# Optimization experiments

Measured on AMD Instinct MI355X. Metric: run time of the kernel, lower is better.

The kernel has to match this reference:

```python
import jax, jax.numpy as jnp
import numpy as np
import math

H = 16
D_MODEL = 1024
D_K = D_MODEL // H


def setup_inputs() -> dict:
    key = jax.random.key(0)
    ks = jax.random.split(key, 11)
    B, S = 2, 2048
    scale = 1.0 / math.sqrt(D_MODEL)
    inp = {
        "query": jax.random.normal(ks[0], (B, S, D_MODEL), dtype=jnp.float32),
        "key": jax.random.normal(ks[1], (B, S, D_MODEL), dtype=jnp.float32),
        "value": jax.random.normal(ks[2], (B, S, D_MODEL), dtype=jnp.float32),
        # torch nn.Linear convention: W is [out_features, in_features]
        "Wq": jax.random.normal(ks[3], (D_MODEL, D_MODEL), dtype=jnp.float32) * scale,
        "bq": jnp.zeros((D_MODEL,), dtype=jnp.float32),
        "Wk": jax.random.normal(ks[4], (D_MODEL, D_MODEL), dtype=jnp.float32) * scale,
        "bk": jnp.zeros((D_MODEL,), dtype=jnp.float32),
        "Wv": jax.random.normal(ks[5], (D_MODEL, D_MODEL), dtype=jnp.float32) * scale,
        "bv": jnp.zeros((D_MODEL,), dtype=jnp.float32),
        "Wo": jax.random.normal(ks[6], (D_MODEL, D_MODEL), dtype=jnp.float32) * scale,
        "bo": jnp.zeros((D_MODEL,), dtype=jnp.float32),
    }
    return inp


def _split_heads(x):
    # [b, s, h*d_k] -> [b, h, s, d_k]
    b, s, _ = x.shape
    return x.reshape(b, s, H, D_K).transpose(0, 2, 1, 3)


def reference(query, key, value, Wq, bq, Wk, bk, Wv, bv, Wo, bo):
    q = _split_heads(query @ Wq.T + bq)
    k = _split_heads(key @ Wk.T + bk)
    v = _split_heads(value @ Wv.T + bv)
    # scaled dot-product attention, full L x L scores per head
    scores = jnp.einsum("bhqd,bhkd->bhqk", q, k) / math.sqrt(D_K)
    attn = jax.nn.softmax(scores, axis=-1)
    ctx = jnp.einsum("bhqk,bhkd->bhqd", attn, v)  # [b, h, s, d_k]
    b, h, s, d = ctx.shape
    ctx = ctx.transpose(0, 2, 1, 3).reshape(b, s, h * d)
    return ctx @ Wo.T + bo
```

## Files before the change

kernel.cpp:

```cpp
#include <hip/hip_runtime.h>

typedef unsigned int u32;
typedef unsigned short u16;
typedef __attribute__((ext_vector_type(8))) short short8;
typedef __attribute__((ext_vector_type(4))) float f32x4;
typedef __attribute__((ext_vector_type(2))) u32 u32x2;
typedef __attribute__((ext_vector_type(4))) u32 u32x4;

#define DEV __device__ __forceinline__

DEV u16 f2bf(float f) {
  u32 u = __builtin_bit_cast(u32, f);
  u = (u + 0x7FFFu + ((u >> 16) & 1u)) >> 16;
  return (u16)u;
}

DEV float fexp2(float x) {
#if __has_builtin(__builtin_amdgcn_exp2f)
  return __builtin_amdgcn_exp2f(x);
#else
  return exp2f(x);
#endif
}

DEV u32 cvt_pk_bf16(float lo, float hi) {
  u32 r;
  asm("v_cvt_pk_bf16_f32 %0, %1, %2" : "=v"(r) : "v"(lo), "v"(hi));
  return r;
}

DEV void llds16(const void* g, void* lds) {
  __builtin_amdgcn_global_load_lds(
      (const __attribute__((address_space(1))) u32*)g,
      (__attribute__((address_space(3))) u32*)lds, 16, 0, 0);
}

struct CvtArgs {
  const float* src[7];
  u16* dst[7];
};

__global__ void cvt_all(CvtArgs ca) {
  int i = blockIdx.x * blockDim.x + threadIdx.x;
  int chunk = i >> 17;
  int seg = chunk < 12 ? (chunk >> 2) : (chunk - 9);
  u32 base8 = (seg < 3) ? (u32)seg * 524288u : 1572864u + ((u32)seg - 3) * 131072u;
  size_t off = ((size_t)i - base8) * 8;
  const f32x4* p = (const f32x4*)(ca.src[seg] + off);
  f32x4 a = p[0], b = p[1];
  short8 o;
  o[0] = (short)f2bf(a[0]); o[1] = (short)f2bf(a[1]);
  o[2] = (short)f2bf(a[2]); o[3] = (short)f2bf(a[3]);
  o[4] = (short)f2bf(b[0]); o[5] = (short)f2bf(b[1]);
  o[6] = (short)f2bf(b[2]); o[7] = (short)f2bf(b[3]);
  *(short8*)(ca.dst[seg] + off) = o;
}

struct GemmArgs {
  const u16* A[3];
  const u16* W[3];
  const float* bias[3];
  void* C[3];
  float scale[3];
};

template <int BM, int BN, int WAVES_M, int OUT_BF16, int NB_M>
__global__ __launch_bounds__(256, 2) void gemm_bt(GemmArgs ga) {
  constexpr int K = 1024, N = 1024;
  constexpr int WAVES_N = 4 / WAVES_M;
  constexpr int WM = BM / WAVES_M, WN = BN / WAVES_N;
  constexpr int AM = WM / 16, AN = WN / 16;
  constexpr int SEGS = (BM + BN) / 16;
  constexpr int PW = SEGS / 4;

  __shared__ u16 lsA[BM * 32];
  __shared__ u16 lsB[BN * 32];

  const u32 orig = blockIdx.x;
  const u32 nid = (orig & 7u) * (gridDim.x >> 3) + (orig >> 3);
  const int bn = (int)(nid & 7u);
  const int bm = (int)((nid >> 3) % (u32)NB_M);
  const int z = (int)((nid >> 3) / (u32)NB_M);

  const u16* __restrict__ A = ga.A[z];
  const u16* __restrict__ W = ga.W[z];
  const int tid = threadIdx.x;
  const int l = tid & 63, w = tid >> 6;
  const int lg = l >> 4, lr = l & 15;
  const int wm = w / WAVES_N, wn = w % WAVES_N;

  f32x4 acc[AM][AN];
#pragma unroll
  for (int i = 0; i < AM; ++i)
#pragma unroll
    for (int j = 0; j < AN; ++j) acc[i][j] = (f32x4){0.f, 0.f, 0.f, 0.f};

  for (int k0 = 0; k0 < K; k0 += 32) {
    __syncthreads();
#pragma unroll
    for (int i = 0; i < PW; ++i) {
      int s = w * PW + i;
      if (s < BM / 16) {
        u32 sb = s * 1024;
        u32 lb = sb + l * 16;
        u32 row = lb >> 6, colS = (lb & 63) >> 1;
        llds16(A + (size_t)(bm * BM + row) * K + k0 + colS, (char*)lsA + sb);
      } else {
        u32 sb = (u32)(s - BM / 16) * 1024;
        u32 lb = sb + l * 16;
        u32 row = lb >> 6, colS = (lb & 63) >> 1;
        llds16(W + (size_t)(bn * BN + row) * K + k0 + colS, (char*)lsB + sb);
      }
    }
    __syncthreads();
    short8 af[AM], bf[AN];
#pragma unroll
    for (int i = 0; i < AM; ++i)
      af[i] = *(const short8*)&lsA[(wm * WM + i * 16 + lr) * 32 + lg * 8];
#pragma unroll
    for (int j = 0; j < AN; ++j)
      bf[j] = *(const short8*)&lsB[(wn * WN + j * 16 + lr) * 32 + lg * 8];
#pragma unroll
    for (int i = 0; i < AM; ++i)
#pragma unroll
      for (int j = 0; j < AN; ++j)
        acc[i][j] = __builtin_amdgcn_mfma_f32_16x16x32_bf16(af[i], bf[j], acc[i][j], 0, 0, 0);
  }

  const float sc = ga.scale[z];
  const float* __restrict__ bias = ga.bias[z];
#pragma unroll
  for (int j = 0; j < AN; ++j) {
    int col = bn * BN + wn * WN + j * 16 + lr;
    float bv = bias[col];
#pragma unroll
    for (int i = 0; i < AM; ++i) {
      int row0 = bm * BM + wm * WM + i * 16 + lg * 4;
#pragma unroll
      for (int r = 0; r < 4; ++r) {
        float v = (acc[i][j][r] + bv) * sc;
        if constexpr (OUT_BF16)
          ((u16*)ga.C[z])[(size_t)(row0 + r) * N + col] = f2bf(v);
        else
          ((float*)ga.C[z])[(size_t)(row0 + r) * N + col] = v;
      }
    }
  }
}

__global__ __launch_bounds__(256, 2) void attn_fwd(
    const u16* __restrict__ Q, const u16* __restrict__ Kp,
    const u16* __restrict__ V, u16* __restrict__ O) {
  constexpr int S = 2048, LD = 1024;
  __shared__ u16 Kt[4][64 * 64];
  __shared__ u16 Vt[4][64 * 64];
  const int tid = threadIdx.x;
  const int l = tid & 63, w = tid >> 6;
  const int lg = l >> 4, lr = l & 15;

  const u32 orig = blockIdx.x;
  const u32 nid = (orig & 7u) * 64u + (orig >> 3);
  const int qt = (int)(nid & 15u);
  const int h = (int)((nid >> 4) & 15u);
  const int b = (int)(nid >> 8);

  const size_t base = ((size_t)b * S) * LD + h * 64;
  const int q0 = qt * 128 + w * 32;

  short8 qf[2][2];
#pragma unroll
  for (int g = 0; g < 2; ++g)
#pragma unroll
    for (int c = 0; c < 2; ++c)
      qf[g][c] = *(const short8*)&Q[base + (size_t)(q0 + g * 16 + lr) * LD + c * 32 + lg * 8];

  f32x4 acc[2][4];
#pragma unroll
  for (int g = 0; g < 2; ++g)
#pragma unroll
    for (int i = 0; i < 4; ++i) acc[g][i] = (f32x4){0.f, 0.f, 0.f, 0.f};
  float lsum[2] = {0.f, 0.f};

  const int m = tid & 31;
  const int kp0 = m * 2;
  const int key0 = ((m & 16) << 1) + ((m & 2) << 3) + (((m >> 2) & 3) << 2) + ((m & 1) << 1);
  const int vd0 = (tid >> 5) * 8;

#define KSTAGE(T)                                                               \
  {                                                                             \
    _Pragma("unroll") for (int i_ = 0; i_ < 2; ++i_) {                          \
      u32 sb = (u32)(w * 2 + i_) * 1024;                                        \
      u32 lb = sb + l * 16;                                                     \
      u32 key = lb >> 7;                                                        \
      u32 inner = (lb & 127) ^ ((key & 7) << 4);                                \
      llds16(Kp + base + (size_t)((T) * 64 + key) * LD + (inner >> 1),          \
             (char*)Kt[(T) & 3] + sb);                                          \
    }                                                                           \
  }
#define VLOAD(T, VA, VB)                                                        \
  {                                                                             \
    VA = *(const short8*)&V[base + (size_t)((T) * 64 + key0) * LD + vd0];       \
    VB = *(const short8*)&V[base + (size_t)((T) * 64 + key0 + 1) * LD + vd0];   \
  }
#define VWRITE(T, VA, VB)                                                       \
  {                                                                             \
    _Pragma("unroll") for (int jj = 0; jj < 8; ++jj) {                          \
      u32 pv = (u32)(u16)(VA)[jj] | ((u32)(u16)(VB)[jj] << 16);                 \
      u32 addr = (u32)((vd0 + jj) * 128 + kp0 * 2) ^ ((u32)jj << 4);            \
      *(u32*)((char*)Vt[(T) & 3] + addr) = pv;                                  \
    }                                                                           \
  }
#define QK(T, SV)                                                               \
  {                                                                             \
    __builtin_amdgcn_s_setprio(1);                                              \
    _Pragma("unroll") for (int ks = 0; ks < 4; ++ks) {                          \
      u32 a0 = (u32)(((ks * 16 + lr) * 128 + lg * 16) ^ ((lr & 7) << 4));       \
      short8 kf0 = *(const short8*)((const char*)Kt[(T) & 3] + a0);             \
      short8 kf1 = *(const short8*)((const char*)Kt[(T) & 3] + (a0 ^ 64));      \
      _Pragma("unroll") for (int g = 0; g < 2; ++g) {                           \
        f32x4 s_ = (f32x4){0.f, 0.f, 0.f, 0.f};                                 \
        s_ = __builtin_amdgcn_mfma_f32_16x16x32_bf16(kf0, qf[g][0], s_, 0, 0, 0); \
        s_ = __builtin_amdgcn_mfma_f32_16x16x32_bf16(kf1, qf[g][1], s_, 0, 0, 0); \
        SV[g][ks] = s_;                                                         \
      }                                                                         \
    }                                                                           \
    __builtin_amdgcn_s_setprio(0);                                              \
  }
#define SM(SV, PK)                                                              \
  {                                                                             \
    _Pragma("unroll") for (int g = 0; g < 2; ++g) {                             \
      _Pragma("unroll") for (int ks = 0; ks < 4; ++ks) {                        \
        float e0 = fexp2(SV[g][ks][0]), e1 = fexp2(SV[g][ks][1]);               \
        float e2 = fexp2(SV[g][ks][2]), e3 = fexp2(SV[g][ks][3]);               \
        lsum[g] += (e0 + e1) + (e2 + e3);                                       \
        PK[g][ks * 2 + 0] = cvt_pk_bf16(e0, e1);                                \
        PK[g][ks * 2 + 1] = cvt_pk_bf16(e2, e3);                                \
      }                                                                         \
    }                                                                           \
  }
#define PV(T, PK)                                                               \
  {                                                                             \
    __builtin_amdgcn_s_setprio(1);                                              \
    _Pragma("unroll") for (int ds = 0; ds < 4; ++ds) {                          \
      _Pragma("unroll") for (int c = 0; c < 2; ++c) {                           \
        u32 va_ = (u32)(((ds * 16 + lr) * 128 + c * 64 + lg * 16) ^ ((lr & 7) << 4)); \
        short8 vf = *(const short8*)((const char*)Vt[(T) & 3] + va_);           \
        _Pragma("unroll") for (int g = 0; g < 2; ++g) {                         \
          u32x4 pc = {PK[g][c * 4 + 0], PK[g][c * 4 + 1], PK[g][c * 4 + 2], PK[g][c * 4 + 3]}; \
          short8 pf = __builtin_bit_cast(short8, pc);                           \
          acc[g][ds] = __builtin_amdgcn_mfma_f32_16x16x32_bf16(vf, pf, acc[g][ds], 0, 0, 0); \
        }                                                                       \
      }                                                                         \
    }                                                                           \
    __builtin_amdgcn_s_setprio(0);                                              \
  }
#define ITER(t, SVC, SVN, VCA, VCB, VNA, VNB)                                   \
  {                                                                             \
    if ((t) < 30) { VLOAD((t) + 2, VNA, VNB); KSTAGE((t) + 2); }                \
    if ((t) < 31) QK((t) + 1, SVN);                                             \
    u32 pk_[2][8];                                                              \
    SM(SVC, pk_);                                                               \
    if ((t) < 31) VWRITE((t) + 1, VCA, VCB);                                    \
    PV(t, pk_);                                                                 \
    __syncthreads();                                                            \
  }

  f32x4 svA[2][4], svB[2][4];
  short8 vaA, vbA, vaB, vbB;

  VLOAD(0, vaB, vbB); KSTAGE(0);
  VLOAD(1, vaA, vbA); KSTAGE(1);
  VWRITE(0, vaB, vbB);
  __syncthreads();
  QK(0, svA);

  for (int tt = 0; tt < 16; ++tt) {
    ITER(2 * tt, svA, svB, vaA, vbA, vaB, vbB);
    ITER(2 * tt + 1, svB, svA, vaB, vbB, vaA, vbA);
  }

#pragma unroll
  for (int g = 0; g < 2; ++g) {
    lsum[g] += __shfl_xor(lsum[g], 16);
    lsum[g] += __shfl_xor(lsum[g], 32);
  }
#pragma unroll
  for (int g = 0; g < 2; ++g) {
    float inv = __builtin_amdgcn_rcpf(lsum[g]);
#pragma unroll
    for (int ds = 0; ds < 4; ++ds) {
      u32x2 ov;
      ov[0] = cvt_pk_bf16(acc[g][ds][0] * inv, acc[g][ds][1] * inv);
      ov[1] = cvt_pk_bf16(acc[g][ds][2] * inv, acc[g][ds][3] * inv);
      *(u32x2*)&O[base + (size_t)(q0 + g * 16 + lr) * LD + ds * 16 + lg * 4] = ov;
    }
  }
#undef KSTAGE
#undef VLOAD
#undef VWRITE
#undef QK
#undef SM
#undef PV
#undef ITER
}

extern "C" void kernel_launch(void* const* d_in, const int* in_sizes, int n_in,
                              void* d_out, int out_size, void* d_ws, size_t ws_size,
                              hipStream_t stream) {
  constexpr size_t SZ_X = 4096ull * 1024;
  constexpr size_t SZ_W = 1024ull * 1024;
  const float* bq = (const float*)d_in[4];
  const float* bk = (const float*)d_in[6];
  const float* bv = (const float*)d_in[8];
  const float* bo = (const float*)d_in[10];

  char* ws = (char*)d_ws;
  u16* xq = (u16*)ws;
  u16* xk = xq + SZ_X;
  u16* xv = xk + SZ_X;
  u16* wqb = xv + SZ_X;
  u16* wkb = wqb + SZ_W;
  u16* wvb = wkb + SZ_W;
  u16* wob = wvb + SZ_W;
  u16* Qp = wob + SZ_W;
  u16* Kp = Qp + SZ_X;
  u16* Vp = Kp + SZ_X;
  u16* Cx = Vp + SZ_X;

  CvtArgs ca;
  ca.src[0] = (const float*)d_in[0]; ca.dst[0] = xq;
  ca.src[1] = (const float*)d_in[1]; ca.dst[1] = xk;
  ca.src[2] = (const float*)d_in[2]; ca.dst[2] = xv;
  ca.src[3] = (const float*)d_in[3]; ca.dst[3] = wqb;
  ca.src[4] = (const float*)d_in[5]; ca.dst[4] = wkb;
  ca.src[5] = (const float*)d_in[7]; ca.dst[5] = wvb;
  ca.src[6] = (const float*)d_in[9]; ca.dst[6] = wob;
  cvt_all<<<dim3(8192), 256, 0, stream>>>(ca);

  GemmArgs g1;
  g1.A[0] = xq;  g1.A[1] = xk;  g1.A[2] = xv;
  g1.W[0] = wqb; g1.W[1] = wkb; g1.W[2] = wvb;
  g1.bias[0] = bq; g1.bias[1] = bk; g1.bias[2] = bv;
  g1.C[0] = Qp; g1.C[1] = Kp; g1.C[2] = Vp;
  g1.scale[0] = 0.18033688011112042f;
  g1.scale[1] = 1.f; g1.scale[2] = 1.f;
  gemm_bt<128, 128, 2, 1, 32><<<dim3(768), 256, 0, stream>>>(g1);

  attn_fwd<<<dim3(512), 256, 0, stream>>>(Qp, Kp, Vp, Cx);

  GemmArgs g2 = {};
  g2.A[0] = Cx; g2.W[0] = wob; g2.bias[0] = bo; g2.C[0] = d_out; g2.scale[0] = 1.f;
  gemm_bt<64, 128, 1, 0, 64><<<dim3(512), 256, 0, stream>>>(g2);
}
```

Before: 127.2 us.

## Load K tiles directly into registers instead of staging through LDS

K fragments are now read from global memory straight into per-wave registers, double-buffered in registers, instead of being copied into a 4-deep shared-memory ring and then read back. The V shared buffer shrinks from four stages to two. This removes the LDS round trip for K and cuts shared memory use, which could allow more resident blocks. In exchange, each wave independently loads the full K tile from global/L2 (four times the redundant traffic per block), and register pressure grows by 16 short8 values, which risks spills under launch_bounds(256,2).

```diff
diff --git a/kernel.cpp b/kernel.cpp
--- a/kernel.cpp
+++ b/kernel.cpp
@@ -152,8 +152,7 @@
     const u16* __restrict__ Q, const u16* __restrict__ Kp,
     const u16* __restrict__ V, u16* __restrict__ O) {
   constexpr int S = 2048, LD = 1024;
-  __shared__ u16 Kt[4][64 * 64];
-  __shared__ u16 Vt[4][64 * 64];
+  __shared__ u16 Vt[2][64 * 64];
   const int tid = threadIdx.x;
   const int l = tid & 63, w = tid >> 6;
   const int lg = l >> 4, lr = l & 15;
@@ -186,16 +185,11 @@
   const int key0 = ((m & 16) << 1) + ((m & 2) << 3) + (((m >> 2) & 3) << 2) + ((m & 1) << 1);
   const int vd0 = (tid >> 5) * 8;
 
-#define KSTAGE(T)                                                               \
-  {                                                                             \
-    _Pragma("unroll") for (int i_ = 0; i_ < 2; ++i_) {                          \
-      u32 sb = (u32)(w * 2 + i_) * 1024;                                        \
-      u32 lb = sb + l * 16;                                                     \
-      u32 key = lb >> 7;                                                        \
-      u32 inner = (lb & 127) ^ ((key & 7) << 4);                                \
-      llds16(Kp + base + (size_t)((T) * 64 + key) * LD + (inner >> 1),          \
-             (char*)Kt[(T) & 3] + sb);                                          \
-    }                                                                           \
+#define KLOAD(T, KF)                                                            \
+  {                                                                             \
+    _Pragma("unroll") for (int ks = 0; ks < 4; ++ks)                            \
+    _Pragma("unroll") for (int c = 0; c < 2; ++c)                               \
+      KF[ks][c] = *(const short8*)&Kp[base + (size_t)((T) * 64 + ks * 16 + lr) * LD + c * 32 + lg * 8]; \
   }
 #define VLOAD(T, VA, VB)                                                        \
   {                                                                             \
@@ -207,20 +201,17 @@
     _Pragma("unroll") for (int jj = 0; jj < 8; ++jj) {                          \
       u32 pv = (u32)(u16)(VA)[jj] | ((u32)(u16)(VB)[jj] << 16);                 \
       u32 addr = (u32)((vd0 + jj) * 128 + kp0 * 2) ^ ((u32)jj << 4);            \
-      *(u32*)((char*)Vt[(T) & 3] + addr) = pv;                                  \
+      *(u32*)((char*)Vt[(T) & 1] + addr) = pv;                                  \
     }                                                                           \
   }
-#define QK(T, SV)                                                               \
+#define QK(KF, SV)                                                              \
   {                                                                             \
     __builtin_amdgcn_s_setprio(1);                                              \
     _Pragma("unroll") for (int ks = 0; ks < 4; ++ks) {                          \
-      u32 a0 = (u32)(((ks * 16 + lr) * 128 + lg * 16) ^ ((lr & 7) << 4));       \
-      short8 kf0 = *(const short8*)((const char*)Kt[(T) & 3] + a0);             \
-      short8 kf1 = *(const short8*)((const char*)Kt[(T) & 3] + (a0 ^ 64));      \
       _Pragma("unroll") for (int g = 0; g < 2; ++g) {                           \
         f32x4 s_ = (f32x4){0.f, 0.f, 0.f, 0.f};                                 \
-        s_ = __builtin_amdgcn_mfma_f32_16x16x32_bf16(kf0, qf[g][0], s_, 0, 0, 0); \
-        s_ = __builtin_amdgcn_mfma_f32_16x16x32_bf16(kf1, qf[g][1], s_, 0, 0, 0); \
+        s_ = __builtin_amdgcn_mfma_f32_16x16x32_bf16(KF[ks][0], qf[g][0], s_, 0, 0, 0); \
+        s_ = __builtin_amdgcn_mfma_f32_16x16x32_bf16(KF[ks][1], qf[g][1], s_, 0, 0, 0); \
         SV[g][ks] = s_;                                                         \
       }                                                                         \
     }                                                                           \
@@ -244,7 +235,7 @@
     _Pragma("unroll") for (int ds = 0; ds < 4; ++ds) {                          \
       _Pragma("unroll") for (int c = 0; c < 2; ++c) {                           \
         u32 va_ = (u32)(((ds * 16 + lr) * 128 + c * 64 + lg * 16) ^ ((lr & 7) << 4)); \
-        short8 vf = *(const short8*)((const char*)Vt[(T) & 3] + va_);           \
+        short8 vf = *(const short8*)((const char*)Vt[(T) & 1] + va_);           \
         _Pragma("unroll") for (int g = 0; g < 2; ++g) {                         \
           u32x4 pc = {PK[g][c * 4 + 0], PK[g][c * 4 + 1], PK[g][c * 4 + 2], PK[g][c * 4 + 3]}; \
           short8 pf = __builtin_bit_cast(short8, pc);                           \
@@ -254,10 +245,10 @@
     }                                                                           \
     __builtin_amdgcn_s_setprio(0);                                              \
   }
-#define ITER(t, SVC, SVN, VCA, VCB, VNA, VNB)                                   \
-  {                                                                             \
-    if ((t) < 30) { VLOAD((t) + 2, VNA, VNB); KSTAGE((t) + 2); }                \
-    if ((t) < 31) QK((t) + 1, SVN);                                             \
+#define ITER(t, SVC, SVN, KFC, KFN, VCA, VCB, VNA, VNB)                         \
+  {                                                                             \
+    if ((t) < 30) { VLOAD((t) + 2, VNA, VNB); KLOAD((t) + 2, KFN); }            \
+    if ((t) < 31) QK(KFC, SVN);                                                 \
     u32 pk_[2][8];                                                              \
     SM(SVC, pk_);                                                               \
     if ((t) < 31) VWRITE((t) + 1, VCA, VCB);                                    \
@@ -266,17 +257,20 @@
   }
 
   f32x4 svA[2][4], svB[2][4];
+  short8 kfA[4][2], kfB[4][2];
   short8 vaA, vbA, vaB, vbB;
 
-  VLOAD(0, vaB, vbB); KSTAGE(0);
-  VLOAD(1, vaA, vbA); KSTAGE(1);
+  KLOAD(0, kfA);
+  KLOAD(1, kfB);
+  VLOAD(0, vaB, vbB);
+  VLOAD(1, vaA, vbA);
   VWRITE(0, vaB, vbB);
   __syncthreads();
-  QK(0, svA);
+  QK(kfA, svA);
 
   for (int tt = 0; tt < 16; ++tt) {
-    ITER(2 * tt, svA, svB, vaA, vbA, vaB, vbB);
-    ITER(2 * tt + 1, svB, svA, vaB, vbB, vaA, vbA);
+    ITER(2 * tt, svA, svB, kfB, kfA, vaA, vbA, vaB, vbB);
+    ITER(2 * tt + 1, svB, svA, kfA, kfB, vaB, vbB, vaA, vbA);
   }
 
 #pragma unroll
@@ -295,7 +289,7 @@
       *(u32x2*)&O[base + (size_t)(q0 + g * 16 + lr) * LD + ds * 16 + lg * 4] = ov;
     }
   }
-#undef KSTAGE
+#undef KLOAD
 #undef VLOAD
 #undef VWRITE
 #undef QK
```

New measurement: 151.7 us. +19.3%, slower.

## Fuse activation fp32-to-bf16 conversion into QKV projection GEMM tile loads

Applied to the files above, without the earlier changes.

Drops the separate pre-pass that converted the three fp32 activation tensors to bf16. The QKV GEMM now reads fp32 A tiles straight from global memory into registers, packs them with v_cvt_pk_bf16 and writes them to LDS. The weight-only conversion kernel also switches to the packed convert instruction. This saves a full write and reread of the bf16 activation copies, but the GEMM's A loads become twice as wide and go through registers instead of direct-to-LDS loads, so their latency may be more exposed in the unpipelined k-loop.

```diff
diff --git a/kernel.cpp b/kernel.cpp
--- a/kernel.cpp
+++ b/kernel.cpp
@@ -35,43 +35,39 @@
       (__attribute__((address_space(3))) u32*)lds, 16, 0, 0);
 }
 
-struct CvtArgs {
-  const float* src[7];
-  u16* dst[7];
+struct CvtW {
+  const float* src[4];
+  u16* dst[4];
 };
 
-__global__ void cvt_all(CvtArgs ca) {
+__global__ void cvt_w(CvtW cw) {
   int i = blockIdx.x * blockDim.x + threadIdx.x;
-  int chunk = i >> 17;
-  int seg = chunk < 12 ? (chunk >> 2) : (chunk - 9);
-  u32 base8 = (seg < 3) ? (u32)seg * 524288u : 1572864u + ((u32)seg - 3) * 131072u;
-  size_t off = ((size_t)i - base8) * 8;
-  const f32x4* p = (const f32x4*)(ca.src[seg] + off);
+  int seg = i >> 17;
+  size_t off = ((size_t)(i & 131071)) * 8;
+  const f32x4* p = (const f32x4*)(cw.src[seg] + off);
   f32x4 a = p[0], b = p[1];
-  short8 o;
-  o[0] = (short)f2bf(a[0]); o[1] = (short)f2bf(a[1]);
-  o[2] = (short)f2bf(a[2]); o[3] = (short)f2bf(a[3]);
-  o[4] = (short)f2bf(b[0]); o[5] = (short)f2bf(b[1]);
-  o[6] = (short)f2bf(b[2]); o[7] = (short)f2bf(b[3]);
-  *(short8*)(ca.dst[seg] + off) = o;
+  u32x4 o;
+  o[0] = cvt_pk_bf16(a[0], a[1]);
+  o[1] = cvt_pk_bf16(a[2], a[3]);
+  o[2] = cvt_pk_bf16(b[0], b[1]);
+  o[3] = cvt_pk_bf16(b[2], b[3]);
+  *(u32x4*)(cw.dst[seg] + off) = o;
 }
 
 struct GemmArgs {
-  const u16* A[3];
+  const void* A[3];
   const u16* W[3];
   const float* bias[3];
   void* C[3];
   float scale[3];
 };
 
-template <int BM, int BN, int WAVES_M, int OUT_BF16, int NB_M>
+template <int BM, int BN, int WAVES_M, int OUT_BF16, int NB_M, int A_F32>
 __global__ __launch_bounds__(256, 2) void gemm_bt(GemmArgs ga) {
   constexpr int K = 1024, N = 1024;
   constexpr int WAVES_N = 4 / WAVES_M;
   constexpr int WM = BM / WAVES_M, WN = BN / WAVES_N;
   constexpr int AM = WM / 16, AN = WN / 16;
-  constexpr int SEGS = (BM + BN) / 16;
-  constexpr int PW = SEGS / 4;
 
   __shared__ u16 lsA[BM * 32];
   __shared__ u16 lsB[BN * 32];
@@ -82,7 +78,6 @@
   const int bm = (int)((nid >> 3) % (u32)NB_M);
   const int z = (int)((nid >> 3) / (u32)NB_M);
 
-  const u16* __restrict__ A = ga.A[z];
   const u16* __restrict__ W = ga.W[z];
   const int tid = threadIdx.x;
   const int l = tid & 63, w = tid >> 6;
@@ -97,19 +92,47 @@
 
   for (int k0 = 0; k0 < K; k0 += 32) {
     __syncthreads();
-#pragma unroll
-    for (int i = 0; i < PW; ++i) {
-      int s = w * PW + i;
-      if (s < BM / 16) {
-        u32 sb = s * 1024;
-        u32 lb = sb + l * 16;
-        u32 row = lb >> 6, colS = (lb & 63) >> 1;
-        llds16(A + (size_t)(bm * BM + row) * K + k0 + colS, (char*)lsA + sb);
-      } else {
-        u32 sb = (u32)(s - BM / 16) * 1024;
+    if constexpr (A_F32) {
+      const float* __restrict__ Af = (const float*)ga.A[z];
+#pragma unroll
+      for (int i = 0; i < BN / 64; ++i) {
+        u32 sb = (u32)(w * (BN / 64) + i) * 1024;
         u32 lb = sb + l * 16;
         u32 row = lb >> 6, colS = (lb & 63) >> 1;
         llds16(W + (size_t)(bn * BN + row) * K + k0 + colS, (char*)lsB + sb);
+      }
+      {
+        constexpr int TPR = 256 / BM;
+        int row = tid / TPR, kh = tid % TPR;
+        const f32x4* src = (const f32x4*)(Af + (size_t)(bm * BM + row) * K + k0 + kh * 16);
+        f32x4 f0 = src[0], f1 = src[1], f2 = src[2], f3 = src[3];
+        u32x4 o0, o1;
+        o0[0] = cvt_pk_bf16(f0[0], f0[1]); o0[1] = cvt_pk_bf16(f0[2], f0[3]);
+        o0[2] = cvt_pk_bf16(f1[0], f1[1]); o0[3] = cvt_pk_bf16(f1[2], f1[3]);
+        o1[0] = cvt_pk_bf16(f2[0], f2[1]); o1[1] = cvt_pk_bf16(f2[2], f2[3]);
+        o1[2] = cvt_pk_bf16(f3[0], f3[1]); o1[3] = cvt_pk_bf16(f3[2], f3[3]);
+        char* dst = (char*)lsA + row * 64 + kh * 32;
+        *(u32x4*)dst = o0;
+        *(u32x4*)(dst + 16) = o1;
+      }
+    } else {
+      const u16* __restrict__ A = (const u16*)ga.A[z];
+      constexpr int SEGS = (BM + BN) / 16;
+      constexpr int PW = SEGS / 4;
+#pragma unroll
+      for (int i = 0; i < PW; ++i) {
+        int s = w * PW + i;
+        if (s < BM / 16) {
+          u32 sb = s * 1024;
+          u32 lb = sb + l * 16;
+          u32 row = lb >> 6, colS = (lb & 63) >> 1;
+          llds16(A + (size_t)(bm * BM + row) * K + k0 + colS, (char*)lsA + sb);
+        } else {
+          u32 sb = (u32)(s - BM / 16) * 1024;
+          u32 lb = sb + l * 16;
+          u32 row = lb >> 6, colS = (lb & 63) >> 1;
+          llds16(W + (size_t)(bn * BN + row) * K + k0 + colS, (char*)lsB + sb);
+        }
       }
     }
     __syncthreads();
@@ -315,10 +338,7 @@
   const float* bo = (const float*)d_in[10];
 
   char* ws = (char*)d_ws;
-  u16* xq = (u16*)ws;
-  u16* xk = xq + SZ_X;
-  u16* xv = xk + SZ_X;
-  u16* wqb = xv + SZ_X;
+  u16* wqb = (u16*)ws;
   u16* wkb = wqb + SZ_W;
   u16* wvb = wkb + SZ_W;
   u16* wob = wvb + SZ_W;
@@ -327,28 +347,25 @@
   u16* Vp = Kp + SZ_X;
   u16* Cx = Vp + SZ_X;
 
-  CvtArgs ca;
-  ca.src[0] = (const float*)d_in[0]; ca.dst[0] = xq;
-  ca.src[1] = (const float*)d_in[1]; ca.dst[1] = xk;
-  ca.src[2] = (const float*)d_in[2]; ca.dst[2] = xv;
-  ca.src[3] = (const float*)d_in[3]; ca.dst[3] = wqb;
-  ca.src[4] = (const float*)d_in[5]; ca.dst[4] = wkb;
-  ca.src[5] = (const float*)d_in[7]; ca.dst[5] = wvb;
-  ca.src[6] = (const float*)d_in[9]; ca.dst[6] = wob;
-  cvt_all<<<dim3(8192), 256, 0, stream>>>(ca);
+  CvtW cw;
+  cw.src[0] = (const float*)d_in[3]; cw.dst[0] = wqb;
+  cw.src[1] = (const float*)d_in[5]; cw.dst[1] = wkb;
+  cw.src[2] = (const float*)d_in[7]; cw.dst[2] = wvb;
+  cw.src[3] = (const float*)d_in[9]; cw.dst[3] = wob;
+  cvt_w<<<dim3(2048), 256, 0, stream>>>(cw);
 
   GemmArgs g1;
-  g1.A[0] = xq;  g1.A[1] = xk;  g1.A[2] = xv;
+  g1.A[0] = d_in[0]; g1.A[1] = d_in[1]; g1.A[2] = d_in[2];
   g1.W[0] = wqb; g1.W[1] = wkb; g1.W[2] = wvb;
   g1.bias[0] = bq; g1.bias[1] = bk; g1.bias[2] = bv;
   g1.C[0] = Qp; g1.C[1] = Kp; g1.C[2] = Vp;
   g1.scale[0] = 0.18033688011112042f;
   g1.scale[1] = 1.f; g1.scale[2] = 1.f;
-  gemm_bt<128, 128, 2, 1, 32><<<dim3(768), 256, 0, stream>>>(g1);
+  gemm_bt<128, 128, 2, 1, 32, 1><<<dim3(768), 256, 0, stream>>>(g1);
 
   attn_fwd<<<dim3(512), 256, 0, stream>>>(Qp, Kp, Vp, Cx);
 
   GemmArgs g2 = {};
   g2.A[0] = Cx; g2.W[0] = wob; g2.bias[0] = bo; g2.C[0] = d_out; g2.scale[0] = 1.f;
-  gemm_bt<64, 128, 1, 0, 64><<<dim3(512), 256, 0, stream>>>(g2);
-}
+  gemm_bt<64, 128, 1, 0, 64, 0><<<dim3(512), 256, 0, stream>>>(g2);
+}
```

Result: slower. 131.2 us (+3.2%).
